# Kernel tuning notes

Measured on AMD Instinct MI355X. Metric: run time of the kernel, lower is better.

Reference implementation:

```python
import jax, jax.numpy as jnp
import numpy as np

B, L, E, R, A = 1024, 40, 1024, 1024, 512


def setup_inputs() -> dict:
    key = jax.random.key(0)
    ks = jax.random.split(key, 20)
    s = 0.05  # weight scale to avoid gate saturation
    inp = {
        "xt": jax.random.normal(ks[0], (B, E), jnp.float32),
        "xt_mask": jnp.ones((B, 1), jnp.float32),
        "V": jax.random.normal(ks[1], (B, L, R), jnp.float32),
        "pos_feat": jax.random.normal(ks[2], (B, R), jnp.float32),
        "h1": jax.random.normal(ks[3], (1, B, R), jnp.float32),
        "c1": jax.random.normal(ks[4], (1, B, R), jnp.float32),
        "h2": jax.random.normal(ks[5], (1, B, R), jnp.float32),
        "c2": jax.random.normal(ks[6], (1, B, R), jnp.float32),
        "Wg": jax.random.normal(ks[7], (E, R), jnp.float32) * s,
        "bg": jnp.zeros((R,), jnp.float32),
        "Wi1": jax.random.normal(ks[8], (E, 4 * R), jnp.float32) * s,
        "bi1": jnp.zeros((4 * R,), jnp.float32),
        "Wa1": jax.random.normal(ks[9], (R, 4 * R), jnp.float32) * s,
        "ba1": jnp.zeros((4 * R,), jnp.float32),
        "Wh1": jax.random.normal(ks[10], (R, 4 * R), jnp.float32) * s,
        "bh1": jnp.zeros((4 * R,), jnp.float32),
        "Wi2": jax.random.normal(ks[11], (R, 4 * R), jnp.float32) * s,
        "bi2": jnp.zeros((4 * R,), jnp.float32),
        "Wa2": jax.random.normal(ks[12], (R, 4 * R), jnp.float32) * s,
        "ba2": jnp.zeros((4 * R,), jnp.float32),
        "Wh2": jax.random.normal(ks[13], (R, 4 * R), jnp.float32) * s,
        "bh2": jnp.zeros((4 * R,), jnp.float32),
        "Wv2a": jax.random.normal(ks[14], (R, A), jnp.float32) * s,
        "bv2a": jnp.zeros((A,), jnp.float32),
        "Wh2a": jax.random.normal(ks[15], (2 * R, A), jnp.float32) * s,
        "bh2a": jnp.zeros((A,), jnp.float32),
        "Wa2w": jax.random.normal(ks[16], (A, 1), jnp.float32) * s,
        "ba2w": jnp.zeros((1,), jnp.float32),
    }
    return inp


def _lstm_cell(in1, in2, h, c, Wi, bi, Wa, ba, Wh, bh, mask):
    # all_input_sums: [B, 4R]; torch gate order: i, f, o (sigmoid) then g (tanh)
    s = in1 @ Wi + bi + in2 @ Wa + ba + h @ Wh + bh
    i_g = jax.nn.sigmoid(s[:, 0 * R:1 * R])
    f_g = jax.nn.sigmoid(s[:, 1 * R:2 * R])
    o_g = jax.nn.sigmoid(s[:, 2 * R:3 * R])
    g = jnp.tanh(s[:, 3 * R:4 * R])
    c_new = f_g * c + i_g * g
    c_new = c_new * mask + c * (1.0 - mask)
    h_new = o_g * jnp.tanh(c_new)
    h_new = h_new * mask + h * (1.0 - mask)
    return h_new, c_new


def reference(xt, xt_mask, V, pos_feat, h1, c1, h2, c2,
              Wg, bg, Wi1, bi1, Wa1, ba1, Wh1, bh1,
              Wi2, bi2, Wa2, ba2, Wh2, bh2,
              Wv2a, bv2a, Wh2a, bh2a, Wa2w, ba2w):
    h1l, c1l = h1[-1], c1[-1]  # [B, R]
    h2l, c2l = h2[-1], c2[-1]
    # additive attention over L frames
    hq = jnp.concatenate([h1l, h2l], axis=1) @ Wh2a + bh2a        # [B, A]
    e = jnp.tanh(hq[:, None, :] + V @ Wv2a + bv2a) @ Wa2w + ba2w  # [B, L, 1]
    w = jax.nn.softmax(e, axis=1)                                  # softmax over L
    af = jnp.sum(w * V, axis=1)                                    # [B, R]
    # gate (dropout in eval mode -> identity)
    gate = jax.nn.relu(xt @ Wg + bg)
    gated_pos = gate * pos_feat + pos_feat
    # two-layer LSTM
    out1, c1n = _lstm_cell(xt, gated_pos, h1l, c1l, Wi1, bi1, Wa1, ba1, Wh1, bh1, xt_mask)
    out2, c2n = _lstm_cell(out1, af, h2l, c2l, Wi2, bi2, Wa2, ba2, Wh2, bh2, xt_mask)
    return (out2, out1[None], c1n[None], out2[None], c2n[None])
```

## Files before the change

### kernel.cpp

```cpp
#include <hip/hip_runtime.h>
#include <math.h>

#define BB 1024
#define LL 40
#define RR 1024

using short8 = __attribute__((ext_vector_type(8))) short;
using us8    = __attribute__((ext_vector_type(8))) unsigned short;
using f32x4  = __attribute__((ext_vector_type(4))) float;

__device__ __forceinline__ ushort f2bf(float f) {
    union { float f; unsigned u; } a; a.f = f;
    unsigned r = a.u + 0x7fffu + ((a.u >> 16) & 1u);
    return (ushort)(r >> 16);
}
__device__ __forceinline__ float bf2f(ushort u) {
    union { unsigned u; float f; } a; a.u = ((unsigned)u) << 16;
    return a.f;
}
__device__ __forceinline__ float ftanh(float x) {
    float cx = fminf(fmaxf(x, -15.f), 15.f);
    float e = __expf(2.f * cx);
    return (e - 1.f) / (e + 1.f);
}
__device__ __forceinline__ float fsigmoid(float x) {
    float cx = fminf(fmaxf(x, -30.f), 30.f);
    return 1.f / (1.f + __expf(-cx));
}

__global__ __launch_bounds__(256) void conv_bf16_kernel(
    const float* __restrict__ src, ushort* __restrict__ dst, int n8)
{
    const int i = blockIdx.x * 256 + threadIdx.x;
    if (i >= n8) return;
    const float4* s4 = (const float4*)(src + (size_t)i * 8);
    float4 x = s4[0], y = s4[1];
    us8 v;
    v[0] = f2bf(x.x); v[1] = f2bf(x.y); v[2] = f2bf(x.z); v[3] = f2bf(x.w);
    v[4] = f2bf(y.x); v[5] = f2bf(y.y); v[6] = f2bf(y.z); v[7] = f2bf(y.w);
    ((us8*)dst)[i] = v;
}

struct CP3 { const float* in[3]; ushort* out[3]; };
__global__ __launch_bounds__(256) void conv_bf16_batch3_kernel(CP3 p, int n8)
{
    const int z = blockIdx.y;
    const int i = blockIdx.x * 256 + threadIdx.x;
    if (i >= n8) return;
    const float4* s4 = (const float4*)(p.in[z] + (size_t)i * 8);
    float4 x = s4[0], y = s4[1];
    us8 v;
    v[0] = f2bf(x.x); v[1] = f2bf(x.y); v[2] = f2bf(x.z); v[3] = f2bf(x.w);
    v[4] = f2bf(y.x); v[5] = f2bf(y.y); v[6] = f2bf(y.z); v[7] = f2bf(y.w);
    ((us8*)p.out[z])[i] = v;
}

struct TP6 { const float* in[6]; ushort* out[6]; int N[6]; };
__global__ __launch_bounds__(256) void transpose_conv_kernel(TP6 p)
{
    const int z = blockIdx.z;
    const int Nn = p.N[z];
    const int n0 = blockIdx.x * 64;
    if (n0 >= Nn) return;
    const int k0 = blockIdx.y * 64;
    const float* in = p.in[z];
    ushort* out = p.out[z];

    __shared__ float tile[64][65];
    const int t = threadIdx.x;
    const int tx = t & 63, ty = t >> 6;
#pragma unroll
    for (int r = 0; r < 16; ++r) {
        const int row = ty * 16 + r;
        tile[row][tx] = in[(size_t)(k0 + row) * Nn + n0 + tx];
    }
    __syncthreads();
    const int n = t >> 2, kq = t & 3;
    us8 v0, v1;
#pragma unroll
    for (int j = 0; j < 8; ++j) v0[j] = f2bf(tile[kq * 16 + j][n]);
#pragma unroll
    for (int j = 0; j < 8; ++j) v1[j] = f2bf(tile[kq * 16 + 8 + j][n]);
    ushort* op = out + (size_t)(n0 + n) * 1024 + k0 + kq * 16;
    *(us8*)op = v0;
    *((us8*)op + 1) = v1;
}

template <int NP, int EPI, int SK>
__global__ __launch_bounds__(256) void gemm_bf16(
    const ushort* __restrict__ A0, const ushort* __restrict__ A1, const ushort* __restrict__ A2,
    const ushort* __restrict__ W0, const ushort* __restrict__ W1, const ushort* __restrict__ W2,
    const float* __restrict__ b0, const float* __restrict__ b1, const float* __restrict__ b2,
    float* __restrict__ C, int M, int N,
    const float* __restrict__ hq, const float* __restrict__ bv2a,
    const float* __restrict__ Wa2w, float* __restrict__ epart)
{
    __shared__ ushort Alds[128 * 72];
    __shared__ ushort Blds[128 * 72];
    __shared__ float  red2[128][2];

    const int t = threadIdx.x;
    const int lane = t & 63;
    const int wave = t >> 6;
    const int wm = wave >> 1, wn = wave & 1;

    int bx, by;
    if constexpr (EPI == 2) {
        const int lin = blockIdx.y * 4 + blockIdx.x;
        const int nl = (lin & 7) * 160 + (lin >> 3);
        bx = nl & 3; by = nl >> 2;
    } else {
        bx = blockIdx.x; by = blockIdx.y;
    }
    const int m0 = by * 128, n0 = bx * 128;

    const int srow = t >> 1, skh = t & 1;
    const int soff = srow * 72 + skh * 32;

    f32x4 acc[4][4];
#pragma unroll
    for (int i = 0; i < 4; ++i)
#pragma unroll
        for (int j = 0; j < 4; ++j) acc[i][j] = (f32x4){0.f, 0.f, 0.f, 0.f};

    const int total = NP * 16;
    const int per   = total / SK;
    const int s0    = blockIdx.z * per;
    const int sEnd  = s0 + per;

    short8 ra[4], rw[4];
    {
        const int p  = (NP == 1) ? 0 : (s0 >> 4);
        const int k0 = (s0 & 15) << 6;
        const ushort* Ap = (p == 0) ? A0 : ((p == 1) ? A1 : A2);
        const ushort* Wp = (p == 0) ? W0 : ((p == 1) ? W1 : W2);
        const short8* ag = (const short8*)(Ap + (size_t)(m0 + srow) * 1024 + k0 + skh * 32);
        const short8* wg = (const short8*)(Wp + (size_t)(n0 + srow) * 1024 + k0 + skh * 32);
#pragma unroll
        for (int j = 0; j < 4; ++j) { ra[j] = ag[j]; rw[j] = wg[j]; }
    }

    for (int s = s0; s < sEnd; ++s) {
        __syncthreads();
#pragma unroll
        for (int j = 0; j < 4; ++j) {
            *(short8*)&Alds[soff + j * 8] = ra[j];
            *(short8*)&Blds[soff + j * 8] = rw[j];
        }
        __syncthreads();

        if (s + 1 < sEnd) {
            const int sn = s + 1;
            const int p  = (NP == 1) ? 0 : (sn >> 4);
            const int k0 = (sn & 15) << 6;
            const ushort* Ap = (p == 0) ? A0 : ((p == 1) ? A1 : A2);
            const ushort* Wp = (p == 0) ? W0 : ((p == 1) ? W1 : W2);
            const short8* ag = (const short8*)(Ap + (size_t)(m0 + srow) * 1024 + k0 + skh * 32);
            const short8* wg = (const short8*)(Wp + (size_t)(n0 + srow) * 1024 + k0 + skh * 32);
#pragma unroll
            for (int j = 0; j < 4; ++j) { ra[j] = ag[j]; rw[j] = wg[j]; }
        }

#pragma unroll
        for (int ks = 0; ks < 2; ++ks) {
            short8 aF[4], bF[4];
#pragma unroll
            for (int mi = 0; mi < 4; ++mi)
                aF[mi] = *(const short8*)&Alds[(wm * 64 + mi * 16 + (lane & 15)) * 72 + ks * 32 + (lane >> 4) * 8];
#pragma unroll
            for (int ni = 0; ni < 4; ++ni)
                bF[ni] = *(const short8*)&Blds[(wn * 64 + ni * 16 + (lane & 15)) * 72 + ks * 32 + (lane >> 4) * 8];
#pragma unroll
            for (int mi = 0; mi < 4; ++mi)
#pragma unroll
                for (int ni = 0; ni < 4; ++ni)
                    acc[mi][ni] = __builtin_amdgcn_mfma_f32_16x16x32_bf16(aF[mi], bF[ni], acc[mi][ni], 0, 0, 0);
        }
    }

    if constexpr (EPI == 0) {
#pragma unroll
        for (int ni = 0; ni < 4; ++ni) {
            const int col = n0 + wn * 64 + ni * 16 + (lane & 15);
            float bs = b0[col];
            if (NP > 1) bs += b1[col];
            if (NP > 2) bs += b2[col];
#pragma unroll
            for (int mi = 0; mi < 4; ++mi) {
                const int row = m0 + wm * 64 + mi * 16 + ((lane >> 4) << 2);
#pragma unroll
                for (int r = 0; r < 4; ++r)
                    C[(size_t)(row + r) * N + col] = acc[mi][ni][r] + bs;
            }
        }
    } else if constexpr (EPI == 3) {
        float* Cz = C + (size_t)blockIdx.z * M * N;
#pragma unroll
        for (int ni = 0; ni < 4; ++ni) {
            const int col = n0 + wn * 64 + ni * 16 + (lane & 15);
#pragma unroll
            for (int mi = 0; mi < 4; ++mi) {
                const int row = m0 + wm * 64 + mi * 16 + ((lane >> 4) << 2);
#pragma unroll
                for (int r = 0; r < 4; ++r)
                    Cz[(size_t)(row + r) * N + col] = acc[mi][ni][r];
            }
        }
    } else if constexpr (EPI == 2) {
        float wa[4], bv[4];
        int coln[4];
#pragma unroll
        for (int ni = 0; ni < 4; ++ni) {
            coln[ni] = n0 + wn * 64 + ni * 16 + (lane & 15);
            wa[ni] = Wa2w[coln[ni]];
            bv[ni] = bv2a[coln[ni]];
        }
#pragma unroll
        for (int mi = 0; mi < 4; ++mi) {
            const int rowb = m0 + wm * 64 + mi * 16 + ((lane >> 4) << 2);
#pragma unroll
            for (int r = 0; r < 4; ++r) {
                const int row = rowb + r;
                const int b = row / LL;
                float v = 0.f;
#pragma unroll
                for (int ni = 0; ni < 4; ++ni) {
                    float x = acc[mi][ni][r] + hq[(size_t)b * 512 + coln[ni]] + bv[ni];
                    v += ftanh(x) * wa[ni];
                }
                v += __shfl_xor(v, 1);
                v += __shfl_xor(v, 2);
                v += __shfl_xor(v, 4);
                v += __shfl_xor(v, 8);
                if ((lane & 15) == 0) red2[rowb - m0 + r][wn] = v;
            }
        }
        __syncthreads();
        if (t < 128)
            epart[(size_t)(m0 + t) * 4 + bx] = red2[t][0] + red2[t][1];
    }
}

__global__ __launch_bounds__(256) void reduce_hq_kernel(
    const float* __restrict__ part, const float* __restrict__ bias, float* __restrict__ hq)
{
    const int i = blockIdx.x * 256 + threadIdx.x;
    float s = bias[i & 511];
#pragma unroll
    for (int z = 0; z < 8; ++z) s += part[(size_t)z * 524288 + i];
    hq[i] = s;
}

__global__ __launch_bounds__(256) void reduce_gate_kernel(
    const float* __restrict__ part, const float* __restrict__ bias,
    const float* __restrict__ pos, ushort* __restrict__ gpb)
{
    const int i = blockIdx.x * 256 + threadIdx.x;
    float s = bias[i & 1023];
#pragma unroll
    for (int z = 0; z < 4; ++z) s += part[(size_t)z * 1048576 + i];
    const float g = fmaxf(s, 0.f);
    gpb[i] = f2bf(g * pos[i] + pos[i]);
}

__global__ __launch_bounds__(256) void softmax_af_kernel(
    const float* __restrict__ epart, const ushort* __restrict__ Vb,
    const float* __restrict__ ba2w, ushort* __restrict__ afb)
{
    const int b = blockIdx.x;
    const int tid = threadIdx.x;
    __shared__ float e_raw[LL];
    __shared__ float e_exp[LL];

    if (tid < LL) {
        const float* ep = &epart[(size_t)(b * LL + tid) * 4];
        float e = ba2w[0];
#pragma unroll
        for (int c = 0; c < 4; ++c) e += ep[c];
        e_raw[tid] = e;
    }
    __syncthreads();
    float mx = -1e30f;
#pragma unroll
    for (int l = 0; l < LL; ++l) mx = fmaxf(mx, e_raw[l]);
    if (tid < LL) e_exp[tid] = __expf(e_raw[tid] - mx);
    __syncthreads();
    float sum = 0.f;
#pragma unroll
    for (int l = 0; l < LL; ++l) sum += e_exp[l];
    const float inv = 1.f / sum;

    const int r4 = tid * 4;
    const ushort* vp = &Vb[(size_t)b * LL * RR + r4];
    float a0 = 0.f, a1 = 0.f, a2 = 0.f, a3 = 0.f;
#pragma unroll 8
    for (int l = 0; l < LL; ++l) {
        ushort4 v = *(const ushort4*)&vp[(size_t)l * RR];
        const float w = e_exp[l];
        a0 += w * bf2f(v.x); a1 += w * bf2f(v.y);
        a2 += w * bf2f(v.z); a3 += w * bf2f(v.w);
    }
    ushort* op = &afb[(size_t)b * RR + r4];
    op[0] = f2bf(a0 * inv); op[1] = f2bf(a1 * inv);
    op[2] = f2bf(a2 * inv); op[3] = f2bf(a3 * inv);
}

__global__ __launch_bounds__(256) void lstm_finish_kernel(
    const float* __restrict__ s, const float* __restrict__ c_in,
    const float* __restrict__ h_in, const float* __restrict__ mask,
    float* __restrict__ h_out, float* __restrict__ h_out2,
    float* __restrict__ c_out, ushort* __restrict__ h_bf)
{
    const int i = blockIdx.x * 256 + threadIdx.x;
    const int b = i >> 10;
    const int r = i & 1023;
    const float* sb = &s[(size_t)b * 4 * RR];
    const float ig = fsigmoid(sb[r]);
    const float fg = fsigmoid(sb[RR + r]);
    const float og = fsigmoid(sb[2 * RR + r]);
    const float g  = ftanh(sb[3 * RR + r]);
    const float m = mask[b];
    const float c = c_in[i];
    float cn = fg * c + ig * g;
    cn = cn * m + c * (1.f - m);
    const float h = h_in[i];
    float hn = og * ftanh(cn);
    hn = hn * m + h * (1.f - m);
    h_out[i] = hn;
    if (h_out2) h_out2[i] = hn;
    c_out[i] = cn;
    if (h_bf) h_bf[i] = f2bf(hn);
}

extern "C" void kernel_launch(void* const* d_in, const int* in_sizes, int n_in,
                              void* d_out, int out_size, void* d_ws, size_t ws_size,
                              hipStream_t stream) {
    const float* xt   = (const float*)d_in[0];
    const float* mask = (const float*)d_in[1];
    const float* V    = (const float*)d_in[2];
    const float* pos  = (const float*)d_in[3];
    const float* h1   = (const float*)d_in[4];
    const float* c1   = (const float*)d_in[5];
    const float* h2   = (const float*)d_in[6];
    const float* c2   = (const float*)d_in[7];
    const float* Wg   = (const float*)d_in[8];
    const float* bg   = (const float*)d_in[9];
    const float* Wi1  = (const float*)d_in[10];
    const float* bi1  = (const float*)d_in[11];
    const float* Wa1  = (const float*)d_in[12];
    const float* ba1  = (const float*)d_in[13];
    const float* Wh1  = (const float*)d_in[14];
    const float* bh1  = (const float*)d_in[15];
    const float* Wi2  = (const float*)d_in[16];
    const float* bi2  = (const float*)d_in[17];
    const float* Wa2  = (const float*)d_in[18];
    const float* ba2  = (const float*)d_in[19];
    const float* Wh2  = (const float*)d_in[20];
    const float* bh2  = (const float*)d_in[21];
    const float* Wv2a = (const float*)d_in[22];
    const float* bv2a = (const float*)d_in[23];
    const float* Wh2a = (const float*)d_in[24];
    const float* bh2a = (const float*)d_in[25];
    const float* Wa2w = (const float*)d_in[26];
    const float* ba2w = (const float*)d_in[27];

    float* out = (float*)d_out;
    float* out2  = out;
    float* out1  = out + (size_t)BB * RR;
    float* c1n   = out + 2 * (size_t)BB * RR;
    float* out2b = out + 3 * (size_t)BB * RR;
    float* c2n   = out + 4 * (size_t)BB * RR;

    ushort* wsu = (ushort*)d_ws;
    size_t o = 0;
    ushort* Vb     = wsu + o; o += (size_t)40960 * 1024;
    ushort* Wh2aT0 = wsu + o; o += (size_t)512 * 1024;
    ushort* Wh2aT1 = wsu + o; o += (size_t)512 * 1024;
    ushort* WgT    = wsu + o; o += (size_t)1024 * 1024;
    ushort* Wv2aT  = wsu + o; o += (size_t)512 * 1024;
    ushort* Wi1T   = wsu + o; o += (size_t)4096 * 1024;
    ushort* Wa1T   = wsu + o; o += (size_t)4096 * 1024;
    ushort* Wh1T   = wsu + o; o += (size_t)4096 * 1024;
    ushort* Wi2T   = wsu + o; o += (size_t)4096 * 1024;
    ushort* Wa2T   = wsu + o; o += (size_t)4096 * 1024;
    ushort* Wh2T   = wsu + o; o += (size_t)4096 * 1024;
    ushort* xtb    = wsu + o; o += (size_t)1024 * 1024;
    ushort* h1b    = wsu + o; o += (size_t)1024 * 1024;
    ushort* h2b    = wsu + o; o += (size_t)1024 * 1024;
    ushort* gpb    = wsu + o; o += (size_t)1024 * 1024;
    ushort* afb    = wsu + o; o += (size_t)1024 * 1024;
    ushort* out1b  = wsu + o; o += (size_t)1024 * 1024;
    float* wsf   = (float*)(wsu + o);
    float* hqf   = wsf;
    float* epart = hqf + 524288;
    float* sbuf  = epart + 163840;
    float* partK = sbuf;

    const dim3 blk(256);

    conv_bf16_kernel<<<dim3(20480), blk, 0, stream>>>(V, Vb, 5242880);
    {
        CP3 p; p.in[0] = xt; p.in[1] = h1; p.in[2] = h2;
        p.out[0] = xtb; p.out[1] = h1b; p.out[2] = h2b;
        conv_bf16_batch3_kernel<<<dim3(512, 3), blk, 0, stream>>>(p, 131072);
    }
    {
        TP6 p;
        p.in[0] = Wi1; p.in[1] = Wa1; p.in[2] = Wh1;
        p.in[3] = Wi2; p.in[4] = Wa2; p.in[5] = Wh2;
        p.out[0] = Wi1T; p.out[1] = Wa1T; p.out[2] = Wh1T;
        p.out[3] = Wi2T; p.out[4] = Wa2T; p.out[5] = Wh2T;
        for (int z = 0; z < 6; ++z) p.N[z] = 4096;
        transpose_conv_kernel<<<dim3(64, 16, 6), blk, 0, stream>>>(p);
    }
    {
        TP6 p;
        p.in[0] = Wh2a; p.in[1] = Wh2a + (size_t)1024 * 512;
        p.in[2] = Wg;   p.in[3] = Wv2a;
        p.out[0] = Wh2aT0; p.out[1] = Wh2aT1; p.out[2] = WgT; p.out[3] = Wv2aT;
        p.N[0] = 512; p.N[1] = 512; p.N[2] = 1024; p.N[3] = 512;
        p.in[4] = nullptr; p.in[5] = nullptr; p.out[4] = nullptr; p.out[5] = nullptr;
        p.N[4] = 0; p.N[5] = 0;
        transpose_conv_kernel<<<dim3(16, 16, 4), blk, 0, stream>>>(p);
    }

    gemm_bf16<2, 3, 8><<<dim3(4, 8, 8), blk, 0, stream>>>(
        h1b, h2b, nullptr, Wh2aT0, Wh2aT1, nullptr,
        nullptr, nullptr, nullptr, partK, 1024, 512, nullptr, nullptr, nullptr, nullptr);
    reduce_hq_kernel<<<dim3(2048), blk, 0, stream>>>(partK, bh2a, hqf);

    gemm_bf16<1, 3, 4><<<dim3(8, 8, 4), blk, 0, stream>>>(
        xtb, nullptr, nullptr, WgT, nullptr, nullptr,
        nullptr, nullptr, nullptr, partK, 1024, 1024, nullptr, nullptr, nullptr, nullptr);
    reduce_gate_kernel<<<dim3(4096), blk, 0, stream>>>(partK, bg, pos, gpb);

    gemm_bf16<1, 2, 1><<<dim3(4, 320, 1), blk, 0, stream>>>(
        Vb, nullptr, nullptr, Wv2aT, nullptr, nullptr,
        nullptr, nullptr, nullptr, nullptr, 40960, 512, hqf, bv2a, Wa2w, epart);
    softmax_af_kernel<<<dim3(BB), blk, 0, stream>>>(epart, Vb, ba2w, afb);

    gemm_bf16<3, 0, 1><<<dim3(32, 8, 1), blk, 0, stream>>>(
        xtb, gpb, h1b, Wi1T, Wa1T, Wh1T, bi1, ba1, bh1,
        sbuf, 1024, 4096, nullptr, nullptr, nullptr, nullptr);
    lstm_finish_kernel<<<dim3(4096), blk, 0, stream>>>(sbuf, c1, h1, mask, out1, nullptr, c1n, out1b);

    gemm_bf16<3, 0, 1><<<dim3(32, 8, 1), blk, 0, stream>>>(
        out1b, afb, h2b, Wi2T, Wa2T, Wh2T, bi2, ba2, bh2,
        sbuf, 1024, 4096, nullptr, nullptr, nullptr, nullptr);
    lstm_finish_kernel<<<dim3(4096), blk, 0, stream>>>(sbuf, c2, h2, mask, out2, out2b, c2n, nullptr);
}
```

Baseline: 323.2 us.

## Fuse fp32-to-bf16 V conversion into a double-buffered 256x256 attention GEMM

Removes the standalone pass that converts V to bf16. The attention-score GEMM now loads fp32 V directly and converts it while staging into LDS, using larger 256x256 tiles with 512 threads. The softmax/context kernel reads fp32 V as well. All GEMMs switch to double-buffered LDS with a single barrier per k-step and raised wave priority around the MFMA loop. This cuts total V traffic and one launch, but the softmax now reads twice the bytes per element and the large-tile kernel uses far more LDS, which lowers occupancy.

```diff
diff --git a/kernel.cpp b/kernel.cpp
--- a/kernel.cpp
+++ b/kernel.cpp
@@ -26,19 +26,6 @@
 __device__ __forceinline__ float fsigmoid(float x) {
     float cx = fminf(fmaxf(x, -30.f), 30.f);
     return 1.f / (1.f + __expf(-cx));
-}
-
-__global__ __launch_bounds__(256) void conv_bf16_kernel(
-    const float* __restrict__ src, ushort* __restrict__ dst, int n8)
-{
-    const int i = blockIdx.x * 256 + threadIdx.x;
-    if (i >= n8) return;
-    const float4* s4 = (const float4*)(src + (size_t)i * 8);
-    float4 x = s4[0], y = s4[1];
-    us8 v;
-    v[0] = f2bf(x.x); v[1] = f2bf(x.y); v[2] = f2bf(x.z); v[3] = f2bf(x.w);
-    v[4] = f2bf(y.x); v[5] = f2bf(y.y); v[6] = f2bf(y.z); v[7] = f2bf(y.w);
-    ((us8*)dst)[i] = v;
 }
 
 struct CP3 { const float* in[3]; ushort* out[3]; };
@@ -86,108 +73,130 @@
     *((us8*)op + 1) = v1;
 }
 
-template <int NP, int EPI, int SK>
-__global__ __launch_bounds__(256) void gemm_bf16(
-    const ushort* __restrict__ A0, const ushort* __restrict__ A1, const ushort* __restrict__ A2,
+template <int BM, int BN, int WM, int WN, bool CVTA, int NP, int EPI, int SK>
+__global__ __launch_bounds__(WM * WN * 64, 2) void gemm_dbuf(
+    const void* __restrict__ A0v, const void* __restrict__ A1v, const void* __restrict__ A2v,
     const ushort* __restrict__ W0, const ushort* __restrict__ W1, const ushort* __restrict__ W2,
     const float* __restrict__ b0, const float* __restrict__ b1, const float* __restrict__ b2,
     float* __restrict__ C, int M, int N,
     const float* __restrict__ hq, const float* __restrict__ bv2a,
     const float* __restrict__ Wa2w, float* __restrict__ epart)
 {
-    __shared__ ushort Alds[128 * 72];
-    __shared__ ushort Blds[128 * 72];
-    __shared__ float  red2[128][2];
-
-    const int t = threadIdx.x;
-    const int lane = t & 63;
-    const int wave = t >> 6;
-    const int wm = wave >> 1, wn = wave & 1;
+    constexpr int PMW = BM / WM, PNW = BN / WN;
+    constexpr int FM = PMW / 16, FN = PNW / 16;
+    __shared__ ushort Alds[2][BM * 72];
+    __shared__ ushort Blds[2][BN * 72];
+
+    const int t = threadIdx.x, lane = t & 63, wave = t >> 6;
+    const int wm = wave / WN, wn = wave % WN;
 
     int bx, by;
     if constexpr (EPI == 2) {
-        const int lin = blockIdx.y * 4 + blockIdx.x;
-        const int nl = (lin & 7) * 160 + (lin >> 3);
-        bx = nl & 3; by = nl >> 2;
+        const int lin = blockIdx.y * gridDim.x + blockIdx.x;
+        const int swz = (lin & 7) * 40 + (lin >> 3);
+        bx = swz & 1; by = swz >> 1;
     } else {
         bx = blockIdx.x; by = blockIdx.y;
     }
-    const int m0 = by * 128, n0 = bx * 128;
+    const int m0 = by * BM, n0 = bx * BN;
 
     const int srow = t >> 1, skh = t & 1;
     const int soff = srow * 72 + skh * 32;
 
-    f32x4 acc[4][4];
-#pragma unroll
-    for (int i = 0; i < 4; ++i)
-#pragma unroll
-        for (int j = 0; j < 4; ++j) acc[i][j] = (f32x4){0.f, 0.f, 0.f, 0.f};
+    f32x4 acc[FM][FN];
+#pragma unroll
+    for (int i = 0; i < FM; ++i)
+#pragma unroll
+        for (int j = 0; j < FN; ++j) acc[i][j] = (f32x4){0.f, 0.f, 0.f, 0.f};
+
+    short8 ra[4]; float4 raf[8]; short8 rw[4];
+
+    auto loadAB = [&](int s) {
+        const int p  = (NP == 1) ? 0 : (s >> 4);
+        const int k0 = (s & 15) << 6;
+        if constexpr (CVTA) {
+            const float* Ap = (const float*)((p == 0) ? A0v : ((p == 1) ? A1v : A2v));
+            const float4* ag = (const float4*)(Ap + (size_t)(m0 + srow) * 1024 + k0 + skh * 32);
+#pragma unroll
+            for (int j = 0; j < 8; ++j) raf[j] = ag[j];
+        } else {
+            const ushort* Ap = (const ushort*)((p == 0) ? A0v : ((p == 1) ? A1v : A2v));
+            const short8* ag = (const short8*)(Ap + (size_t)(m0 + srow) * 1024 + k0 + skh * 32);
+#pragma unroll
+            for (int j = 0; j < 4; ++j) ra[j] = ag[j];
+        }
+        const ushort* Wp = (p == 0) ? W0 : ((p == 1) ? W1 : W2);
+        const short8* wg = (const short8*)(Wp + (size_t)(n0 + srow) * 1024 + k0 + skh * 32);
+#pragma unroll
+        for (int j = 0; j < 4; ++j) rw[j] = wg[j];
+    };
+
+    auto stageTo = [&](int buf) {
+        ushort* ad = &Alds[buf][soff];
+        if constexpr (CVTA) {
+#pragma unroll
+            for (int q = 0; q < 4; ++q) {
+                float4 x = raf[2 * q], y = raf[2 * q + 1];
+                short8 v;
+                v[0] = (short)f2bf(x.x); v[1] = (short)f2bf(x.y);
+                v[2] = (short)f2bf(x.z); v[3] = (short)f2bf(x.w);
+                v[4] = (short)f2bf(y.x); v[5] = (short)f2bf(y.y);
+                v[6] = (short)f2bf(y.z); v[7] = (short)f2bf(y.w);
+                *(short8*)(ad + q * 8) = v;
+            }
+        } else {
+#pragma unroll
+            for (int j = 0; j < 4; ++j) *(short8*)(ad + j * 8) = ra[j];
+        }
+        ushort* bd = &Blds[buf][soff];
+#pragma unroll
+        for (int j = 0; j < 4; ++j) *(short8*)(bd + j * 8) = rw[j];
+    };
 
     const int total = NP * 16;
     const int per   = total / SK;
     const int s0    = blockIdx.z * per;
     const int sEnd  = s0 + per;
 
-    short8 ra[4], rw[4];
-    {
-        const int p  = (NP == 1) ? 0 : (s0 >> 4);
-        const int k0 = (s0 & 15) << 6;
-        const ushort* Ap = (p == 0) ? A0 : ((p == 1) ? A1 : A2);
-        const ushort* Wp = (p == 0) ? W0 : ((p == 1) ? W1 : W2);
-        const short8* ag = (const short8*)(Ap + (size_t)(m0 + srow) * 1024 + k0 + skh * 32);
-        const short8* wg = (const short8*)(Wp + (size_t)(n0 + srow) * 1024 + k0 + skh * 32);
-#pragma unroll
-        for (int j = 0; j < 4; ++j) { ra[j] = ag[j]; rw[j] = wg[j]; }
-    }
-
+    loadAB(s0);
+    stageTo(0);
+    __syncthreads();
+
+    int cur = 0;
     for (int s = s0; s < sEnd; ++s) {
+        if (s + 1 < sEnd) loadAB(s + 1);
+#pragma unroll
+        for (int ks = 0; ks < 2; ++ks) {
+            short8 aF[FM], bF[FN];
+#pragma unroll
+            for (int mi = 0; mi < FM; ++mi)
+                aF[mi] = *(const short8*)&Alds[cur][(wm * PMW + mi * 16 + (lane & 15)) * 72 + ks * 32 + (lane >> 4) * 8];
+#pragma unroll
+            for (int ni = 0; ni < FN; ++ni)
+                bF[ni] = *(const short8*)&Blds[cur][(wn * PNW + ni * 16 + (lane & 15)) * 72 + ks * 32 + (lane >> 4) * 8];
+            __builtin_amdgcn_s_setprio(1);
+#pragma unroll
+            for (int mi = 0; mi < FM; ++mi)
+#pragma unroll
+                for (int ni = 0; ni < FN; ++ni)
+                    acc[mi][ni] = __builtin_amdgcn_mfma_f32_16x16x32_bf16(aF[mi], bF[ni], acc[mi][ni], 0, 0, 0);
+            __builtin_amdgcn_s_setprio(0);
+        }
+        if (s + 1 < sEnd) stageTo(cur ^ 1);
         __syncthreads();
-#pragma unroll
-        for (int j = 0; j < 4; ++j) {
-            *(short8*)&Alds[soff + j * 8] = ra[j];
-            *(short8*)&Blds[soff + j * 8] = rw[j];
-        }
-        __syncthreads();
-
-        if (s + 1 < sEnd) {
-            const int sn = s + 1;
-            const int p  = (NP == 1) ? 0 : (sn >> 4);
-            const int k0 = (sn & 15) << 6;
-            const ushort* Ap = (p == 0) ? A0 : ((p == 1) ? A1 : A2);
-            const ushort* Wp = (p == 0) ? W0 : ((p == 1) ? W1 : W2);
-            const short8* ag = (const short8*)(Ap + (size_t)(m0 + srow) * 1024 + k0 + skh * 32);
-            const short8* wg = (const short8*)(Wp + (size_t)(n0 + srow) * 1024 + k0 + skh * 32);
-#pragma unroll
-            for (int j = 0; j < 4; ++j) { ra[j] = ag[j]; rw[j] = wg[j]; }
-        }
-
-#pragma unroll
-        for (int ks = 0; ks < 2; ++ks) {
-            short8 aF[4], bF[4];
-#pragma unroll
-            for (int mi = 0; mi < 4; ++mi)
-                aF[mi] = *(const short8*)&Alds[(wm * 64 + mi * 16 + (lane & 15)) * 72 + ks * 32 + (lane >> 4) * 8];
-#pragma unroll
-            for (int ni = 0; ni < 4; ++ni)
-                bF[ni] = *(const short8*)&Blds[(wn * 64 + ni * 16 + (lane & 15)) * 72 + ks * 32 + (lane >> 4) * 8];
-#pragma unroll
-            for (int mi = 0; mi < 4; ++mi)
-#pragma unroll
-                for (int ni = 0; ni < 4; ++ni)
-                    acc[mi][ni] = __builtin_amdgcn_mfma_f32_16x16x32_bf16(aF[mi], bF[ni], acc[mi][ni], 0, 0, 0);
-        }
+        cur ^= 1;
     }
 
     if constexpr (EPI == 0) {
 #pragma unroll
-        for (int ni = 0; ni < 4; ++ni) {
-            const int col = n0 + wn * 64 + ni * 16 + (lane & 15);
+        for (int ni = 0; ni < FN; ++ni) {
+            const int col = n0 + wn * PNW + ni * 16 + (lane & 15);
             float bs = b0[col];
             if (NP > 1) bs += b1[col];
             if (NP > 2) bs += b2[col];
 #pragma unroll
-            for (int mi = 0; mi < 4; ++mi) {
-                const int row = m0 + wm * 64 + mi * 16 + ((lane >> 4) << 2);
+            for (int mi = 0; mi < FM; ++mi) {
+                const int row = m0 + wm * PMW + mi * 16 + ((lane >> 4) << 2);
 #pragma unroll
                 for (int r = 0; r < 4; ++r)
                     C[(size_t)(row + r) * N + col] = acc[mi][ni][r] + bs;
@@ -196,35 +205,37 @@
     } else if constexpr (EPI == 3) {
         float* Cz = C + (size_t)blockIdx.z * M * N;
 #pragma unroll
-        for (int ni = 0; ni < 4; ++ni) {
-            const int col = n0 + wn * 64 + ni * 16 + (lane & 15);
-#pragma unroll
-            for (int mi = 0; mi < 4; ++mi) {
-                const int row = m0 + wm * 64 + mi * 16 + ((lane >> 4) << 2);
+        for (int ni = 0; ni < FN; ++ni) {
+            const int col = n0 + wn * PNW + ni * 16 + (lane & 15);
+#pragma unroll
+            for (int mi = 0; mi < FM; ++mi) {
+                const int row = m0 + wm * PMW + mi * 16 + ((lane >> 4) << 2);
 #pragma unroll
                 for (int r = 0; r < 4; ++r)
                     Cz[(size_t)(row + r) * N + col] = acc[mi][ni][r];
             }
         }
     } else if constexpr (EPI == 2) {
-        float wa[4], bv[4];
-        int coln[4];
-#pragma unroll
-        for (int ni = 0; ni < 4; ++ni) {
-            coln[ni] = n0 + wn * 64 + ni * 16 + (lane & 15);
+        __syncthreads();
+        float* red = (float*)&Alds[0][0];
+        float wa[FN], bv[FN];
+        int coln[FN];
+#pragma unroll
+        for (int ni = 0; ni < FN; ++ni) {
+            coln[ni] = n0 + wn * PNW + ni * 16 + (lane & 15);
             wa[ni] = Wa2w[coln[ni]];
             bv[ni] = bv2a[coln[ni]];
         }
 #pragma unroll
-        for (int mi = 0; mi < 4; ++mi) {
-            const int rowb = m0 + wm * 64 + mi * 16 + ((lane >> 4) << 2);
+        for (int mi = 0; mi < FM; ++mi) {
+            const int rowl = wm * PMW + mi * 16 + ((lane >> 4) << 2);
 #pragma unroll
             for (int r = 0; r < 4; ++r) {
-                const int row = rowb + r;
+                const int row = m0 + rowl + r;
                 const int b = row / LL;
                 float v = 0.f;
 #pragma unroll
-                for (int ni = 0; ni < 4; ++ni) {
+                for (int ni = 0; ni < FN; ++ni) {
                     float x = acc[mi][ni][r] + hq[(size_t)b * 512 + coln[ni]] + bv[ni];
                     v += ftanh(x) * wa[ni];
                 }
@@ -232,12 +243,16 @@
                 v += __shfl_xor(v, 2);
                 v += __shfl_xor(v, 4);
                 v += __shfl_xor(v, 8);
-                if ((lane & 15) == 0) red2[rowb - m0 + r][wn] = v;
+                if ((lane & 15) == 0) red[(rowl + r) * WN + wn] = v;
             }
         }
         __syncthreads();
-        if (t < 128)
-            epart[(size_t)(m0 + t) * 4 + bx] = red2[t][0] + red2[t][1];
+        if (t < BM) {
+            float s = 0.f;
+#pragma unroll
+            for (int q = 0; q < WN; ++q) s += red[t * WN + q];
+            epart[(size_t)(m0 + t) * 2 + bx] = s;
+        }
     }
 }
 
@@ -264,7 +279,7 @@
 }
 
 __global__ __launch_bounds__(256) void softmax_af_kernel(
-    const float* __restrict__ epart, const ushort* __restrict__ Vb,
+    const float* __restrict__ epart, const float* __restrict__ V,
     const float* __restrict__ ba2w, ushort* __restrict__ afb)
 {
     const int b = blockIdx.x;
@@ -273,11 +288,8 @@
     __shared__ float e_exp[LL];
 
     if (tid < LL) {
-        const float* ep = &epart[(size_t)(b * LL + tid) * 4];
-        float e = ba2w[0];
-#pragma unroll
-        for (int c = 0; c < 4; ++c) e += ep[c];
-        e_raw[tid] = e;
+        const float* ep = &epart[(size_t)(b * LL + tid) * 2];
+        e_raw[tid] = ba2w[0] + ep[0] + ep[1];
     }
     __syncthreads();
     float mx = -1e30f;
@@ -291,14 +303,13 @@
     const float inv = 1.f / sum;
 
     const int r4 = tid * 4;
-    const ushort* vp = &Vb[(size_t)b * LL * RR + r4];
+    const float* vp = &V[(size_t)b * LL * RR + r4];
     float a0 = 0.f, a1 = 0.f, a2 = 0.f, a3 = 0.f;
 #pragma unroll 8
     for (int l = 0; l < LL; ++l) {
-        ushort4 v = *(const ushort4*)&vp[(size_t)l * RR];
+        float4 v = *(const float4*)&vp[(size_t)l * RR];
         const float w = e_exp[l];
-        a0 += w * bf2f(v.x); a1 += w * bf2f(v.y);
-        a2 += w * bf2f(v.z); a3 += w * bf2f(v.w);
+        a0 += w * v.x; a1 += w * v.y; a2 += w * v.z; a3 += w * v.w;
     }
     ushort* op = &afb[(size_t)b * RR + r4];
     op[0] = f2bf(a0 * inv); op[1] = f2bf(a1 * inv);
@@ -373,7 +384,6 @@
 
     ushort* wsu = (ushort*)d_ws;
     size_t o = 0;
-    ushort* Vb     = wsu + o; o += (size_t)40960 * 1024;
     ushort* Wh2aT0 = wsu + o; o += (size_t)512 * 1024;
     ushort* Wh2aT1 = wsu + o; o += (size_t)512 * 1024;
     ushort* WgT    = wsu + o; o += (size_t)1024 * 1024;
@@ -393,12 +403,12 @@
     float* wsf   = (float*)(wsu + o);
     float* hqf   = wsf;
     float* epart = hqf + 524288;
-    float* sbuf  = epart + 163840;
-    float* partK = sbuf;
+    float* partK = epart + 81920;
+    float* sbuf  = partK + 4194304;
 
     const dim3 blk(256);
-
-    conv_bf16_kernel<<<dim3(20480), blk, 0, stream>>>(V, Vb, 5242880);
+    const dim3 blk8(512);
+
     {
         CP3 p; p.in[0] = xt; p.in[1] = h1; p.in[2] = h2;
         p.out[0] = xtb; p.out[1] = h1b; p.out[2] = h2b;
@@ -424,27 +434,27 @@
         transpose_conv_kernel<<<dim3(16, 16, 4), blk, 0, stream>>>(p);
     }
 
-    gemm_bf16<2, 3, 8><<<dim3(4, 8, 8), blk, 0, stream>>>(
+    gemm_dbuf<128, 128, 2, 2, false, 2, 3, 8><<<dim3(4, 8, 8), blk, 0, stream>>>(
         h1b, h2b, nullptr, Wh2aT0, Wh2aT1, nullptr,
         nullptr, nullptr, nullptr, partK, 1024, 512, nullptr, nullptr, nullptr, nullptr);
     reduce_hq_kernel<<<dim3(2048), blk, 0, stream>>>(partK, bh2a, hqf);
 
-    gemm_bf16<1, 3, 4><<<dim3(8, 8, 4), blk, 0, stream>>>(
+    gemm_dbuf<128, 128, 2, 2, false, 1, 3, 4><<<dim3(8, 8, 4), blk, 0, stream>>>(
         xtb, nullptr, nullptr, WgT, nullptr, nullptr,
         nullptr, nullptr, nullptr, partK, 1024, 1024, nullptr, nullptr, nullptr, nullptr);
     reduce_gate_kernel<<<dim3(4096), blk, 0, stream>>>(partK, bg, pos, gpb);
 
-    gemm_bf16<1, 2, 1><<<dim3(4, 320, 1), blk, 0, stream>>>(
-        Vb, nullptr, nullptr, Wv2aT, nullptr, nullptr,
+    gemm_dbuf<256, 256, 2, 4, true, 1, 2, 1><<<dim3(2, 160, 1), blk8, 0, stream>>>(
+        V, nullptr, nullptr, Wv2aT, nullptr, nullptr,
         nullptr, nullptr, nullptr, nullptr, 40960, 512, hqf, bv2a, Wa2w, epart);
-    softmax_af_kernel<<<dim3(BB), blk, 0, stream>>>(epart, Vb, ba2w, afb);
-
-    gemm_bf16<3, 0, 1><<<dim3(32, 8, 1), blk, 0, stream>>>(
+    softmax_af_kernel<<<dim3(BB), blk, 0, stream>>>(epart, V, ba2w, afb);
+
+    gemm_dbuf<128, 128, 2, 2, false, 3, 0, 1><<<dim3(32, 8, 1), blk, 0, stream>>>(
         xtb, gpb, h1b, Wi1T, Wa1T, Wh1T, bi1, ba1, bh1,
         sbuf, 1024, 4096, nullptr, nullptr, nullptr, nullptr);
     lstm_finish_kernel<<<dim3(4096), blk, 0, stream>>>(sbuf, c1, h1, mask, out1, nullptr, c1n, out1b);
 
-    gemm_bf16<3, 0, 1><<<dim3(32, 8, 1), blk, 0, stream>>>(
+    gemm_dbuf<128, 128, 2, 2, false, 3, 0, 1><<<dim3(32, 8, 1), blk, 0, stream>>>(
         out1b, afb, h2b, Wi2T, Wa2T, Wh2T, bi2, ba2, bh2,
         sbuf, 1024, 4096, nullptr, nullptr, nullptr, nullptr);
     lstm_finish_kernel<<<dim3(4096), blk, 0, stream>>>(sbuf, c2, h2, mask, out2, out2b, c2n, nullptr);
```

New measurement: 623.0 us. +92.7%, slower.

## Fuse attention score GEMM, softmax and context sum; split-K LSTM GEMMs

Applied to the files above, without the earlier changes.

Drops the separate fp32-to-bf16 conversion pass over V. A new fused attention kernel reads fp32 V directly, converts it in registers, computes the score GEMM with MFMA, then does the tanh projection, softmax and weighted sum over L inside one block covering two batch rows. This removes the bf16 V buffer write and re-read and the separate softmax kernel. The LSTM gate GEMMs now use split-K by 2, with biases and partial sums folded into the finish kernel. The cost is a second fp32 read of V for the context sum and larger partial-sum traffic.

```diff
diff --git a/kernel.cpp b/kernel.cpp
--- a/kernel.cpp
+++ b/kernel.cpp
@@ -14,10 +14,6 @@
     unsigned r = a.u + 0x7fffu + ((a.u >> 16) & 1u);
     return (ushort)(r >> 16);
 }
-__device__ __forceinline__ float bf2f(ushort u) {
-    union { unsigned u; float f; } a; a.u = ((unsigned)u) << 16;
-    return a.f;
-}
 __device__ __forceinline__ float ftanh(float x) {
     float cx = fminf(fmaxf(x, -15.f), 15.f);
     float e = __expf(2.f * cx);
@@ -26,19 +22,6 @@
 __device__ __forceinline__ float fsigmoid(float x) {
     float cx = fminf(fmaxf(x, -30.f), 30.f);
     return 1.f / (1.f + __expf(-cx));
-}
-
-__global__ __launch_bounds__(256) void conv_bf16_kernel(
-    const float* __restrict__ src, ushort* __restrict__ dst, int n8)
-{
-    const int i = blockIdx.x * 256 + threadIdx.x;
-    if (i >= n8) return;
-    const float4* s4 = (const float4*)(src + (size_t)i * 8);
-    float4 x = s4[0], y = s4[1];
-    us8 v;
-    v[0] = f2bf(x.x); v[1] = f2bf(x.y); v[2] = f2bf(x.z); v[3] = f2bf(x.w);
-    v[4] = f2bf(y.x); v[5] = f2bf(y.y); v[6] = f2bf(y.z); v[7] = f2bf(y.w);
-    ((us8*)dst)[i] = v;
 }
 
 struct CP3 { const float* in[3]; ushort* out[3]; };
@@ -86,33 +69,20 @@
     *((us8*)op + 1) = v1;
 }
 
-template <int NP, int EPI, int SK>
+template <int NP, int SK>
 __global__ __launch_bounds__(256) void gemm_bf16(
     const ushort* __restrict__ A0, const ushort* __restrict__ A1, const ushort* __restrict__ A2,
     const ushort* __restrict__ W0, const ushort* __restrict__ W1, const ushort* __restrict__ W2,
-    const float* __restrict__ b0, const float* __restrict__ b1, const float* __restrict__ b2,
-    float* __restrict__ C, int M, int N,
-    const float* __restrict__ hq, const float* __restrict__ bv2a,
-    const float* __restrict__ Wa2w, float* __restrict__ epart)
+    float* __restrict__ C, int M, int N)
 {
     __shared__ ushort Alds[128 * 72];
     __shared__ ushort Blds[128 * 72];
-    __shared__ float  red2[128][2];
 
     const int t = threadIdx.x;
     const int lane = t & 63;
     const int wave = t >> 6;
     const int wm = wave >> 1, wn = wave & 1;
-
-    int bx, by;
-    if constexpr (EPI == 2) {
-        const int lin = blockIdx.y * 4 + blockIdx.x;
-        const int nl = (lin & 7) * 160 + (lin >> 3);
-        bx = nl & 3; by = nl >> 2;
-    } else {
-        bx = blockIdx.x; by = blockIdx.y;
-    }
-    const int m0 = by * 128, n0 = bx * 128;
+    const int m0 = blockIdx.y * 128, n0 = blockIdx.x * 128;
 
     const int srow = t >> 1, skh = t & 1;
     const int soff = srow * 72 + skh * 32;
@@ -129,16 +99,18 @@
     const int sEnd  = s0 + per;
 
     short8 ra[4], rw[4];
-    {
-        const int p  = (NP == 1) ? 0 : (s0 >> 4);
-        const int k0 = (s0 & 15) << 6;
+    auto loadAB = [&](int s) {
+        const int p  = (NP == 1) ? 0 : (s >> 4);
+        const int k0 = (s & 15) << 6;
         const ushort* Ap = (p == 0) ? A0 : ((p == 1) ? A1 : A2);
         const ushort* Wp = (p == 0) ? W0 : ((p == 1) ? W1 : W2);
         const short8* ag = (const short8*)(Ap + (size_t)(m0 + srow) * 1024 + k0 + skh * 32);
         const short8* wg = (const short8*)(Wp + (size_t)(n0 + srow) * 1024 + k0 + skh * 32);
 #pragma unroll
         for (int j = 0; j < 4; ++j) { ra[j] = ag[j]; rw[j] = wg[j]; }
-    }
+    };
+
+    loadAB(s0);
 
     for (int s = s0; s < sEnd; ++s) {
         __syncthreads();
@@ -148,19 +120,7 @@
             *(short8*)&Blds[soff + j * 8] = rw[j];
         }
         __syncthreads();
-
-        if (s + 1 < sEnd) {
-            const int sn = s + 1;
-            const int p  = (NP == 1) ? 0 : (sn >> 4);
-            const int k0 = (sn & 15) << 6;
-            const ushort* Ap = (p == 0) ? A0 : ((p == 1) ? A1 : A2);
-            const ushort* Wp = (p == 0) ? W0 : ((p == 1) ? W1 : W2);
-            const short8* ag = (const short8*)(Ap + (size_t)(m0 + srow) * 1024 + k0 + skh * 32);
-            const short8* wg = (const short8*)(Wp + (size_t)(n0 + srow) * 1024 + k0 + skh * 32);
-#pragma unroll
-            for (int j = 0; j < 4; ++j) { ra[j] = ag[j]; rw[j] = wg[j]; }
-        }
-
+        if (s + 1 < sEnd) loadAB(s + 1);
 #pragma unroll
         for (int ks = 0; ks < 2; ++ks) {
             short8 aF[4], bF[4];
@@ -178,66 +138,152 @@
         }
     }
 
-    if constexpr (EPI == 0) {
-#pragma unroll
-        for (int ni = 0; ni < 4; ++ni) {
-            const int col = n0 + wn * 64 + ni * 16 + (lane & 15);
-            float bs = b0[col];
-            if (NP > 1) bs += b1[col];
-            if (NP > 2) bs += b2[col];
-#pragma unroll
-            for (int mi = 0; mi < 4; ++mi) {
-                const int row = m0 + wm * 64 + mi * 16 + ((lane >> 4) << 2);
-#pragma unroll
-                for (int r = 0; r < 4; ++r)
-                    C[(size_t)(row + r) * N + col] = acc[mi][ni][r] + bs;
-            }
-        }
-    } else if constexpr (EPI == 3) {
-        float* Cz = C + (size_t)blockIdx.z * M * N;
-#pragma unroll
-        for (int ni = 0; ni < 4; ++ni) {
-            const int col = n0 + wn * 64 + ni * 16 + (lane & 15);
-#pragma unroll
-            for (int mi = 0; mi < 4; ++mi) {
-                const int row = m0 + wm * 64 + mi * 16 + ((lane >> 4) << 2);
-#pragma unroll
-                for (int r = 0; r < 4; ++r)
-                    Cz[(size_t)(row + r) * N + col] = acc[mi][ni][r];
-            }
-        }
-    } else if constexpr (EPI == 2) {
-        float wa[4], bv[4];
-        int coln[4];
-#pragma unroll
-        for (int ni = 0; ni < 4; ++ni) {
-            coln[ni] = n0 + wn * 64 + ni * 16 + (lane & 15);
-            wa[ni] = Wa2w[coln[ni]];
-            bv[ni] = bv2a[coln[ni]];
-        }
+    float* Cz = C + (size_t)blockIdx.z * M * N;
+#pragma unroll
+    for (int ni = 0; ni < 4; ++ni) {
+        const int col = n0 + wn * 64 + ni * 16 + (lane & 15);
 #pragma unroll
         for (int mi = 0; mi < 4; ++mi) {
-            const int rowb = m0 + wm * 64 + mi * 16 + ((lane >> 4) << 2);
-#pragma unroll
-            for (int r = 0; r < 4; ++r) {
-                const int row = rowb + r;
-                const int b = row / LL;
-                float v = 0.f;
-#pragma unroll
-                for (int ni = 0; ni < 4; ++ni) {
-                    float x = acc[mi][ni][r] + hq[(size_t)b * 512 + coln[ni]] + bv[ni];
-                    v += ftanh(x) * wa[ni];
-                }
-                v += __shfl_xor(v, 1);
-                v += __shfl_xor(v, 2);
-                v += __shfl_xor(v, 4);
-                v += __shfl_xor(v, 8);
-                if ((lane & 15) == 0) red2[rowb - m0 + r][wn] = v;
-            }
-        }
+            const int row = m0 + wm * 64 + mi * 16 + ((lane >> 4) << 2);
+#pragma unroll
+            for (int r = 0; r < 4; ++r)
+                Cz[(size_t)(row + r) * N + col] = acc[mi][ni][r];
+        }
+    }
+}
+
+__global__ __launch_bounds__(512) void attn_fused_kernel(
+    const float* __restrict__ V, const ushort* __restrict__ WT,
+    const float* __restrict__ hq, const float* __restrict__ bv2a,
+    const float* __restrict__ Wa2w, const float* __restrict__ ba2w,
+    ushort* __restrict__ afb)
+{
+    __shared__ ushort Alds[80 * 40];
+    __shared__ ushort Blds[512 * 40];
+
+    const int t = threadIdx.x, lane = t & 63, wn = t >> 6;
+    const int lin = blockIdx.x;
+    const int blk = (lin & 7) * 64 + (lin >> 3);
+    const int m0 = blk * 80;
+
+    f32x4 acc[5][4];
+#pragma unroll
+    for (int i = 0; i < 5; ++i)
+#pragma unroll
+        for (int j = 0; j < 4; ++j) acc[i][j] = (f32x4){0.f, 0.f, 0.f, 0.f};
+
+    const int arow = t >> 2, aq = t & 3;
+
+    float4 raf0, raf1;
+    short8 rw[4];
+    auto loadA = [&](int k0) {
+        const float* ap = V + (size_t)(m0 + arow) * 1024 + k0 + aq * 8;
+        raf0 = ((const float4*)ap)[0];
+        raf1 = ((const float4*)ap)[1];
+    };
+    auto loadB = [&](int k0) {
+        const short8* wp = (const short8*)(WT + (size_t)t * 1024 + k0);
+#pragma unroll
+        for (int j = 0; j < 4; ++j) rw[j] = wp[j];
+    };
+
+    if (t < 320) loadA(0);
+    loadB(0);
+
+    for (int s = 0; s < 32; ++s) {
         __syncthreads();
-        if (t < 128)
-            epart[(size_t)(m0 + t) * 4 + bx] = red2[t][0] + red2[t][1];
+        if (t < 320) {
+            short8 v;
+            v[0] = (short)f2bf(raf0.x); v[1] = (short)f2bf(raf0.y);
+            v[2] = (short)f2bf(raf0.z); v[3] = (short)f2bf(raf0.w);
+            v[4] = (short)f2bf(raf1.x); v[5] = (short)f2bf(raf1.y);
+            v[6] = (short)f2bf(raf1.z); v[7] = (short)f2bf(raf1.w);
+            *(short8*)&Alds[arow * 40 + aq * 8] = v;
+        }
+#pragma unroll
+        for (int j = 0; j < 4; ++j) *(short8*)&Blds[t * 40 + j * 8] = rw[j];
+        __syncthreads();
+        if (s + 1 < 32) {
+            if (t < 320) loadA((s + 1) * 32);
+            loadB((s + 1) * 32);
+        }
+        short8 aF[5], bF[4];
+#pragma unroll
+        for (int mi = 0; mi < 5; ++mi)
+            aF[mi] = *(const short8*)&Alds[(mi * 16 + (lane & 15)) * 40 + (lane >> 4) * 8];
+#pragma unroll
+        for (int ni = 0; ni < 4; ++ni)
+            bF[ni] = *(const short8*)&Blds[(wn * 64 + ni * 16 + (lane & 15)) * 40 + (lane >> 4) * 8];
+        __builtin_amdgcn_s_setprio(1);
+#pragma unroll
+        for (int mi = 0; mi < 5; ++mi)
+#pragma unroll
+            for (int ni = 0; ni < 4; ++ni)
+                acc[mi][ni] = __builtin_amdgcn_mfma_f32_16x16x32_bf16(aF[mi], bF[ni], acc[mi][ni], 0, 0, 0);
+        __builtin_amdgcn_s_setprio(0);
+    }
+
+    __syncthreads();
+    float* red = (float*)Alds;
+    float wa[4], bv[4];
+    int coln[4];
+#pragma unroll
+    for (int ni = 0; ni < 4; ++ni) {
+        coln[ni] = wn * 64 + ni * 16 + (lane & 15);
+        wa[ni] = Wa2w[coln[ni]];
+        bv[ni] = bv2a[coln[ni]];
+    }
+#pragma unroll
+    for (int mi = 0; mi < 5; ++mi) {
+        const int rowb = mi * 16 + ((lane >> 4) << 2);
+#pragma unroll
+        for (int r = 0; r < 4; ++r) {
+            const int row = rowb + r;
+            const int bg = 2 * blk + (row >= 40 ? 1 : 0);
+            float v = 0.f;
+#pragma unroll
+            for (int ni = 0; ni < 4; ++ni)
+                v += ftanh(acc[mi][ni][r] + hq[(size_t)bg * 512 + coln[ni]] + bv[ni]) * wa[ni];
+            v += __shfl_xor(v, 1);
+            v += __shfl_xor(v, 2);
+            v += __shfl_xor(v, 4);
+            v += __shfl_xor(v, 8);
+            if ((lane & 15) == 0) red[row * 8 + wn] = v;
+        }
+    }
+    __syncthreads();
+    float* esm = (float*)Blds;
+    float* wsm = esm + 80;
+    if (t < 80) {
+        float e = ba2w[0];
+#pragma unroll
+        for (int q = 0; q < 8; ++q) e += red[t * 8 + q];
+        esm[t] = e;
+    }
+    __syncthreads();
+    if (t < 80) {
+        const int base = (t >= 40) ? 40 : 0;
+        float mx = -1e30f;
+#pragma unroll
+        for (int l = 0; l < LL; ++l) mx = fmaxf(mx, esm[base + l]);
+        float sum = 0.f;
+#pragma unroll
+        for (int l = 0; l < LL; ++l) sum += __expf(esm[base + l] - mx);
+        wsm[t] = __expf(esm[t] - mx) / sum;
+    }
+    __syncthreads();
+#pragma unroll
+    for (int half = 0; half < 2; ++half) {
+        const int col = t + half * 512;
+        const float* vp = V + (size_t)m0 * 1024 + col;
+        float a0 = 0.f, a1 = 0.f;
+#pragma unroll 4
+        for (int l = 0; l < LL; ++l) {
+            a0 += wsm[l]      * vp[(size_t)l * 1024];
+            a1 += wsm[40 + l] * vp[(size_t)(40 + l) * 1024];
+        }
+        afb[(size_t)(2 * blk) * 1024 + col]     = f2bf(a0);
+        afb[(size_t)(2 * blk + 1) * 1024 + col] = f2bf(a1);
     }
 }
 
@@ -263,65 +309,31 @@
     gpb[i] = f2bf(g * pos[i] + pos[i]);
 }
 
-__global__ __launch_bounds__(256) void softmax_af_kernel(
-    const float* __restrict__ epart, const ushort* __restrict__ Vb,
-    const float* __restrict__ ba2w, ushort* __restrict__ afb)
-{
-    const int b = blockIdx.x;
-    const int tid = threadIdx.x;
-    __shared__ float e_raw[LL];
-    __shared__ float e_exp[LL];
-
-    if (tid < LL) {
-        const float* ep = &epart[(size_t)(b * LL + tid) * 4];
-        float e = ba2w[0];
-#pragma unroll
-        for (int c = 0; c < 4; ++c) e += ep[c];
-        e_raw[tid] = e;
-    }
-    __syncthreads();
-    float mx = -1e30f;
-#pragma unroll
-    for (int l = 0; l < LL; ++l) mx = fmaxf(mx, e_raw[l]);
-    if (tid < LL) e_exp[tid] = __expf(e_raw[tid] - mx);
-    __syncthreads();
-    float sum = 0.f;
-#pragma unroll
-    for (int l = 0; l < LL; ++l) sum += e_exp[l];
-    const float inv = 1.f / sum;
-
-    const int r4 = tid * 4;
-    const ushort* vp = &Vb[(size_t)b * LL * RR + r4];
-    float a0 = 0.f, a1 = 0.f, a2 = 0.f, a3 = 0.f;
-#pragma unroll 8
-    for (int l = 0; l < LL; ++l) {
-        ushort4 v = *(const ushort4*)&vp[(size_t)l * RR];
-        const float w = e_exp[l];
-        a0 += w * bf2f(v.x); a1 += w * bf2f(v.y);
-        a2 += w * bf2f(v.z); a3 += w * bf2f(v.w);
-    }
-    ushort* op = &afb[(size_t)b * RR + r4];
-    op[0] = f2bf(a0 * inv); op[1] = f2bf(a1 * inv);
-    op[2] = f2bf(a2 * inv); op[3] = f2bf(a3 * inv);
-}
-
-__global__ __launch_bounds__(256) void lstm_finish_kernel(
-    const float* __restrict__ s, const float* __restrict__ c_in,
-    const float* __restrict__ h_in, const float* __restrict__ mask,
+__global__ __launch_bounds__(256) void lstm_finish2_kernel(
+    const float* __restrict__ part,
+    const float* __restrict__ bi, const float* __restrict__ ba, const float* __restrict__ bh,
+    const float* __restrict__ c_in, const float* __restrict__ h_in, const float* __restrict__ mask,
     float* __restrict__ h_out, float* __restrict__ h_out2,
     float* __restrict__ c_out, ushort* __restrict__ h_bf)
 {
     const int i = blockIdx.x * 256 + threadIdx.x;
     const int b = i >> 10;
     const int r = i & 1023;
-    const float* sb = &s[(size_t)b * 4 * RR];
-    const float ig = fsigmoid(sb[r]);
-    const float fg = fsigmoid(sb[RR + r]);
-    const float og = fsigmoid(sb[2 * RR + r]);
-    const float g  = ftanh(sb[3 * RR + r]);
+    const float* p0 = part + (size_t)b * 4096;
+    const float* p1 = p0 + 4194304;
+    float sg[4];
+#pragma unroll
+    for (int g = 0; g < 4; ++g) {
+        const int gr = g * 1024 + r;
+        sg[g] = p0[gr] + p1[gr] + bi[gr] + ba[gr] + bh[gr];
+    }
+    const float ig = fsigmoid(sg[0]);
+    const float fg = fsigmoid(sg[1]);
+    const float og = fsigmoid(sg[2]);
+    const float gt = ftanh(sg[3]);
     const float m = mask[b];
     const float c = c_in[i];
-    float cn = fg * c + ig * g;
+    float cn = fg * c + ig * gt;
     cn = cn * m + c * (1.f - m);
     const float h = h_in[i];
     float hn = og * ftanh(cn);
@@ -373,7 +385,6 @@
 
     ushort* wsu = (ushort*)d_ws;
     size_t o = 0;
-    ushort* Vb     = wsu + o; o += (size_t)40960 * 1024;
     ushort* Wh2aT0 = wsu + o; o += (size_t)512 * 1024;
     ushort* Wh2aT1 = wsu + o; o += (size_t)512 * 1024;
     ushort* WgT    = wsu + o; o += (size_t)1024 * 1024;
@@ -392,13 +403,10 @@
     ushort* out1b  = wsu + o; o += (size_t)1024 * 1024;
     float* wsf   = (float*)(wsu + o);
     float* hqf   = wsf;
-    float* epart = hqf + 524288;
-    float* sbuf  = epart + 163840;
-    float* partK = sbuf;
+    float* partK = hqf + 524288;
 
     const dim3 blk(256);
 
-    conv_bf16_kernel<<<dim3(20480), blk, 0, stream>>>(V, Vb, 5242880);
     {
         CP3 p; p.in[0] = xt; p.in[1] = h1; p.in[2] = h2;
         p.out[0] = xtb; p.out[1] = h1b; p.out[2] = h2b;
@@ -424,28 +432,24 @@
         transpose_conv_kernel<<<dim3(16, 16, 4), blk, 0, stream>>>(p);
     }
 
-    gemm_bf16<2, 3, 8><<<dim3(4, 8, 8), blk, 0, stream>>>(
-        h1b, h2b, nullptr, Wh2aT0, Wh2aT1, nullptr,
-        nullptr, nullptr, nullptr, partK, 1024, 512, nullptr, nullptr, nullptr, nullptr);
+    gemm_bf16<2, 8><<<dim3(4, 8, 8), blk, 0, stream>>>(
+        h1b, h2b, nullptr, Wh2aT0, Wh2aT1, nullptr, partK, 1024, 512);
     reduce_hq_kernel<<<dim3(2048), blk, 0, stream>>>(partK, bh2a, hqf);
 
-    gemm_bf16<1, 3, 4><<<dim3(8, 8, 4), blk, 0, stream>>>(
-        xtb, nullptr, nullptr, WgT, nullptr, nullptr,
-        nullptr, nullptr, nullptr, partK, 1024, 1024, nullptr, nullptr, nullptr, nullptr);
+    gemm_bf16<1, 4><<<dim3(8, 8, 4), blk, 0, stream>>>(
+        xtb, nullptr, nullptr, WgT, nullptr, nullptr, partK, 1024, 1024);
     reduce_gate_kernel<<<dim3(4096), blk, 0, stream>>>(partK, bg, pos, gpb);
 
-    gemm_bf16<1, 2, 1><<<dim3(4, 320, 1), blk, 0, stream>>>(
-        Vb, nullptr, nullptr, Wv2aT, nullptr, nullptr,
-        nullptr, nullptr, nullptr, nullptr, 40960, 512, hqf, bv2a, Wa2w, epart);
-    softmax_af_kernel<<<dim3(BB), blk, 0, stream>>>(epart, Vb, ba2w, afb);
-
-    gemm_bf16<3, 0, 1><<<dim3(32, 8, 1), blk, 0, stream>>>(
-        xtb, gpb, h1b, Wi1T, Wa1T, Wh1T, bi1, ba1, bh1,
-        sbuf, 1024, 4096, nullptr, nullptr, nullptr, nullptr);
-    lstm_finish_kernel<<<dim3(4096), blk, 0, stream>>>(sbuf, c1, h1, mask, out1, nullptr, c1n, out1b);
-
-    gemm_bf16<3, 0, 1><<<dim3(32, 8, 1), blk, 0, stream>>>(
-        out1b, afb, h2b, Wi2T, Wa2T, Wh2T, bi2, ba2, bh2,
-        sbuf, 1024, 4096, nullptr, nullptr, nullptr, nullptr);
-    lstm_finish_kernel<<<dim3(4096), blk, 0, stream>>>(sbuf, c2, h2, mask, out2, out2b, c2n, nullptr);
-}
+    attn_fused_kernel<<<dim3(512), dim3(512), 0, stream>>>(
+        V, Wv2aT, hqf, bv2a, Wa2w, ba2w, afb);
+
+    gemm_bf16<3, 2><<<dim3(32, 8, 2), blk, 0, stream>>>(
+        xtb, gpb, h1b, Wi1T, Wa1T, Wh1T, partK, 1024, 4096);
+    lstm_finish2_kernel<<<dim3(4096), blk, 0, stream>>>(
+        partK, bi1, ba1, bh1, c1, h1, mask, out1, nullptr, c1n, out1b);
+
+    gemm_bf16<3, 2><<<dim3(32, 8, 2), blk, 0, stream>>>(
+        out1b, afb, h2b, Wi2T, Wa2T, Wh2T, partK, 1024, 4096);
+    lstm_finish2_kernel<<<dim3(4096), blk, 0, stream>>>(
+        partK, bi2, ba2, bh2, c2, h2, mask, out2, out2b, c2n, nullptr);
+}
```

New measurement: 617.4 us. 1.91x slower.
